# Kernel optimization log

Hardware: AMD Instinct MI355X
Metric: run time of the kernel (lower is better)

## Reference

```python
import jax, jax.numpy as jnp
import numpy as np

N_ATOMS = 4096
HSIZE = 128
N_HEADS = 8
D_K = HSIZE // N_HEADS


def setup_inputs() -> dict:
    key = jax.random.key(0)
    ks = jax.random.split(key, 11)
    s = 1.0 / np.sqrt(HSIZE)
    return {
        "query": jax.random.normal(ks[0], (N_ATOMS, HSIZE), dtype=jnp.float32),
        "key": jax.random.normal(ks[1], (N_ATOMS, HSIZE), dtype=jnp.float32),
        "value": jax.random.normal(ks[2], (N_ATOMS, HSIZE), dtype=jnp.float32),
        "mask": jax.random.randint(ks[3], (N_ATOMS, N_ATOMS), 0, 2, dtype=jnp.int32),
        "Wq": jax.random.normal(ks[4], (HSIZE, HSIZE), dtype=jnp.float32) * s,
        "bq": jnp.zeros((HSIZE,), dtype=jnp.float32),
        "Wk": jax.random.normal(ks[5], (HSIZE, HSIZE), dtype=jnp.float32) * s,
        "bk": jnp.zeros((HSIZE,), dtype=jnp.float32),
        "Wv": jax.random.normal(ks[6], (HSIZE, HSIZE), dtype=jnp.float32) * s,
        "bv": jnp.zeros((HSIZE,), dtype=jnp.float32),
        "Wo": jax.random.normal(ks[7], (HSIZE, HSIZE), dtype=jnp.float32) * s,
    }


def _mha(query, key, value, mask, Wq, bq, Wk, bk, Wv, bv, Wo):
    n = query.shape[0]
    # project and split heads: [n, hsize] -> [H, n, d_k]
    def heads(x, W, b):
        return (x @ W.T + b).reshape(n, N_HEADS, D_K).transpose(1, 0, 2)
    q = heads(query, Wq, bq)
    k = heads(key, Wk, bk)
    v = heads(value, Wv, bv)
    scale = 1.0 / jnp.sqrt(jnp.asarray(D_K, q.dtype))
    scores = jnp.einsum("hnd,hmd->hnm", q, k) * scale  # [H, n, n]
    scores = jnp.where(mask[None, :, :] == 0, jnp.asarray(-1e9, scores.dtype), scores)
    p_attn = jax.nn.softmax(scores, axis=-1)
    x = jnp.einsum("hnm,hmd->hnd", p_attn, v)  # [H, n, d_k]
    x = x.transpose(1, 0, 2).reshape(n, HSIZE)  # merge heads
    return x @ Wo.T  # output_linear has bias=False


def reference(query, key, value, mask, Wq, bq, Wk, bk, Wv, bv, Wo):
    return _mha(query, key, value, mask, Wq, bq, Wk, bk, Wv, bv, Wo)
```

## Files before the change

### kernel.cpp

```cpp
#include <hip/hip_runtime.h>

#define NA 4096
#define HS 128
#define CSTR 136

typedef unsigned short u16;
typedef unsigned long long u64;
using bf16x8  = __attribute__((ext_vector_type(8))) short;
using f32x4   = __attribute__((ext_vector_type(4))) float;
using ushort8 = __attribute__((ext_vector_type(8))) unsigned short;
using u32x4   = __attribute__((ext_vector_type(4))) unsigned;

#define QSCALE 0.18033688011112042f

static __device__ __forceinline__ u16 f2bf(float f) {
    unsigned u = __builtin_bit_cast(unsigned, f);
    u += 0x7FFFu + ((u >> 16) & 1u);
    return (u16)(u >> 16);
}

__global__ __launch_bounds__(256) void cvt_w(
    const float* __restrict__ Wq, const float* __restrict__ Wk,
    const float* __restrict__ Wv, const float* __restrict__ Wo,
    const float* __restrict__ bq, const float* __restrict__ bk,
    const float* __restrict__ bv,
    u16* __restrict__ Wf, float* __restrict__ bb)
{
    const int gid = blockIdx.x * 256 + threadIdx.x;
    const int e = gid * 4;
    const int mat = e >> 14, off = e & 16383;
    const float* src = (mat == 0) ? Wq : (mat == 1) ? Wk : (mat == 2) ? Wv : Wo;
    const float s = (mat == 0) ? QSCALE : 1.0f;
    float4 v = *(const float4*)(src + off);
    ushort4 o;
    o.x = f2bf(v.x * s); o.y = f2bf(v.y * s);
    o.z = f2bf(v.z * s); o.w = f2bf(v.w * s);
    const int j = off >> 7, k0 = off & 127;
    const int j0 = j >> 4, c = j & 15, kk = k0 >> 5, q = (k0 >> 3) & 3;
    const int tgt = mat * 16384 + ((j0 * 4 + kk) * 16 + c) * 32 + q * 8 + (k0 & 7);
    *(ushort4*)(Wf + tgt) = o;
    if (gid < 128)      bb[gid] = bq[gid] * QSCALE;
    else if (gid < 256) bb[gid] = bk[gid - 128];
    else if (gid < 384) bb[gid] = bv[gid - 256];
}

__global__ __launch_bounds__(256) void proj_mfma(
    const float* __restrict__ Xq, const float* __restrict__ Xk, const float* __restrict__ Xv,
    const u16* __restrict__ Wf, const float* __restrict__ bb,
    const int* __restrict__ mask,
    u16* __restrict__ Qbh, u16* __restrict__ Kbh, u16* __restrict__ VtB,
    u64* __restrict__ Mp)
{
    const int blk = blockIdx.x;
    const int t = threadIdx.x;

    if (blk >= 384) {
        const int mb = blk - 384;
        const int wv = t >> 6, lane = t & 63;
        const int row = mb * 4 + wv;
        const int* lp = mask + (size_t)row * NA + lane * 64;
        int4 v[16];
#pragma unroll
        for (int j = 0; j < 16; ++j) v[j] = *(const int4*)(lp + j * 4);
        u64 word = 0;
#pragma unroll
        for (int j = 0; j < 16; ++j) {
            const u64 nib = (u64)((v[j].x != 0 ? 1u : 0u) | (v[j].y != 0 ? 2u : 0u)
                                | (v[j].z != 0 ? 4u : 0u) | (v[j].w != 0 ? 8u : 0u));
            word |= nib << (4 * j);
        }
        Mp[(size_t)row * 64 + lane] = word;
        return;
    }

    const int mat = blk >> 7;
    const float* X = (mat == 0) ? Xq : (mat == 1) ? Xk : Xv;
    const u16* Wm = Wf + mat * 16384;
    const float* bm = bb + mat * 128;
    const int r0b = (blk & 127) * 32;

    __shared__ __align__(16) u16 Xs[32 * CSTR];
    __shared__ __align__(16) u16 Cs[32 * CSTR];

    {
        const int r = t >> 3, cb = (t & 7) * 16;
        const float* Xr = X + (size_t)(r0b + r) * HS + cb;
#pragma unroll
        for (int seg = 0; seg < 4; ++seg) {
            float4 f = *(const float4*)(Xr + seg * 4);
            ushort4 u;
            u.x = f2bf(f.x); u.y = f2bf(f.y); u.z = f2bf(f.z); u.w = f2bf(f.w);
            *(ushort4*)(Xs + r * CSTR + cb + seg * 4) = u;
        }
    }
    __syncthreads();

    const int wv = t >> 6, lane = t & 63;
    const int c = lane & 15, q = lane >> 4;
    const int rw = (wv & 1) * 16;
    const int j0b = (wv >> 1) * 4;

    bf16x8 af[4];
#pragma unroll
    for (int kk = 0; kk < 4; ++kk)
        af[kk] = *(const bf16x8*)(Xs + (rw + c) * CSTR + kk * 32 + q * 8);

    const f32x4 zero = {0.f, 0.f, 0.f, 0.f};
#pragma unroll
    for (int jj = 0; jj < 4; ++jj) {
        const int j0 = j0b + jj;
        f32x4 acc = zero;
#pragma unroll
        for (int kk = 0; kk < 4; ++kk) {
            bf16x8 bf = *(const bf16x8*)(Wm + (j0 * 4 + kk) * 512 + c * 32 + q * 8);
            acc = __builtin_amdgcn_mfma_f32_16x16x32_bf16(af[kk], bf, acc, 0, 0, 0);
        }
        const float bias = bm[j0 * 16 + c];
#pragma unroll
        for (int r = 0; r < 4; ++r)
            Cs[(rw + 4 * q + r) * CSTR + j0 * 16 + c] = f2bf(acc[r] + bias);
    }
    __syncthreads();

    if (mat < 2) {
        u16* dst = (mat == 0) ? Qbh : Kbh;
        const int h8 = t >> 5, r = t & 31;
        const u16* src = Cs + r * CSTR + h8 * 16;
        int drow = r0b + r;
        if (mat == 1) {
            const int k = (r0b & 32) + r;
            const int slot = ((k >> 5) * 2 + ((k >> 2) & 1)) * 16
                           + ((k >> 3) & 3) * 4 + (k & 3);
            drow = (r0b & ~63) + slot;
        }
        u16* dp = dst + (size_t)h8 * (NA * 16) + (size_t)drow * 16;
        *(bf16x8*)(dp)     = *(const bf16x8*)(src);
        *(bf16x8*)(dp + 8) = *(const bf16x8*)(src + 8);
    } else {
        const int d = t >> 1, s = t & 1;
        const int kb = r0b >> 6, ko = (r0b & 32) + s * 16;
        ushort8 v0, v1;
#pragma unroll
        for (int jj = 0; jj < 8; ++jj) v0[jj] = Cs[(s * 16 + jj) * CSTR + d];
#pragma unroll
        for (int jj = 0; jj < 8; ++jj) v1[jj] = Cs[(s * 16 + 8 + jj) * CSTR + d];
        u16* dp = VtB + (size_t)kb * 8192 + d * 64 + ko;
        *(ushort8*)(dp)     = v0;
        *(ushort8*)(dp + 8) = v1;
    }
}

__global__ __launch_bounds__(512, 4) void attn(
    const u64* __restrict__ Mp,
    const u16* __restrict__ Qbh, const u16* __restrict__ Kbh, const u16* __restrict__ VtB,
    float* __restrict__ part)
{
    __shared__ __align__(8)  u64 Mwp[16 * 17];
    __shared__ __align__(8)  u64 Mtab[16];

    const int t = threadIdx.x;
    const int h = t >> 6;
    const int lane = t & 63;
    const int c = lane & 15;
    const int q = lane >> 4;
    const int tile = blockIdx.x, split = blockIdx.y;
    const int i0 = tile * 16;
    const int kt0 = split * 1024;

    if (t < 256) {
        const int row = t >> 4, w = t & 15;
        Mwp[row * 17 + w] = Mp[(size_t)(i0 + row) * 64 + (kt0 >> 6) + w];
    }
    if (t < 16) {
        const unsigned lo = ((t & 1) ? 0xFFFFu : 0u) | ((t & 2) ? 0xFFFF0000u : 0u);
        const unsigned hi = ((t & 4) ? 0xFFFFu : 0u) | ((t & 8) ? 0xFFFF0000u : 0u);
        Mtab[t] = (u64)lo | ((u64)hi << 32);
    }

    const u16* Qh = Qbh + (size_t)h * (NA * 16);
    const u16* Kh = Kbh + (size_t)h * (NA * 16);

    const bf16x8 qf = *(const bf16x8*)(Qh + (size_t)(i0 + c) * 16 + (q & 1) * 8);

    bf16x8 ones;
#pragma unroll
    for (int i = 0; i < 8; ++i) ones[i] = (short)0x3F80;

    __syncthreads();

    const f32x4 zero = {0.f, 0.f, 0.f, 0.f};
    f32x4 Oacc = zero;
    f32x4 Lacc = zero;

    bf16x8 kf[4];
#pragma unroll
    for (int t4 = 0; t4 < 4; ++t4)
        kf[t4] = *(const bf16x8*)(Kh + (size_t)(kt0 + t4 * 16 + c) * 16 + (q & 1) * 8);

#pragma unroll 1
    for (int it = 0; it < 16; ++it) {
        const int kt = kt0 + it * 64;
        const u16* Vb = VtB + (size_t)(kt >> 6) * 8192 + (h * 16 + c) * 64;

        bf16x8 vf0 = *(const bf16x8*)(Vb + q * 8);
        bf16x8 vf1 = *(const bf16x8*)(Vb + 32 + q * 8);

        f32x4 ST[4];
        __builtin_amdgcn_s_setprio(1);
#pragma unroll
        for (int t4 = 0; t4 < 4; ++t4)
            ST[t4] = __builtin_amdgcn_mfma_f32_16x16x32_bf16(kf[t4], qf, zero, 0, 0, 0);
        __builtin_amdgcn_s_setprio(0);

        const int ktn = kt0 + ((it + 1) & 15) * 64;
#pragma unroll
        for (int t4 = 0; t4 < 4; ++t4)
            kf[t4] = *(const bf16x8*)(Kh + (size_t)(ktn + t4 * 16 + c) * 16 + (q & 1) * 8);

        const u64 w = Mwp[c * 17 + it];
        const unsigned wa = (unsigned)(w >> (8 * q));
        const unsigned wb = (unsigned)(w >> (32 + 8 * q));

        unsigned pl[4], ph[4];
#pragma unroll
        for (int t4 = 0; t4 < 4; ++t4) {
            const unsigned nib = (((t4 & 2) ? wb : wa) >> ((t4 & 1) * 4)) & 15u;
            float p0 = __builtin_amdgcn_exp2f(ST[t4][0]);
            float p1 = __builtin_amdgcn_exp2f(ST[t4][1]);
            float p2 = __builtin_amdgcn_exp2f(ST[t4][2]);
            float p3 = __builtin_amdgcn_exp2f(ST[t4][3]);
            unsigned lo, hi;
            asm("v_cvt_pk_bf16_f32 %0, %1, %2" : "=v"(lo) : "v"(p0), "v"(p1));
            asm("v_cvt_pk_bf16_f32 %0, %1, %2" : "=v"(hi) : "v"(p2), "v"(p3));
            const u64 mex = Mtab[nib];
            pl[t4] = lo & (unsigned)mex;
            ph[t4] = hi & (unsigned)(mex >> 32);
        }
        const u32x4 a0 = { pl[0], ph[0], pl[1], ph[1] };
        const u32x4 a1 = { pl[2], ph[2], pl[3], ph[3] };
        const bf16x8 pf0 = __builtin_bit_cast(bf16x8, a0);
        const bf16x8 pf1 = __builtin_bit_cast(bf16x8, a1);

        __builtin_amdgcn_s_setprio(1);
        Oacc = __builtin_amdgcn_mfma_f32_16x16x32_bf16(pf0, vf0, Oacc, 0, 0, 0);
        Oacc = __builtin_amdgcn_mfma_f32_16x16x32_bf16(pf1, vf1, Oacc, 0, 0, 0);
        Lacc = __builtin_amdgcn_mfma_f32_16x16x32_bf16(pf0, ones, Lacc, 0, 0, 0);
        Lacc = __builtin_amdgcn_mfma_f32_16x16x32_bf16(pf1, ones, Lacc, 0, 0, 0);
        __builtin_amdgcn_s_setprio(0);
    }

    float* base = part + (size_t)((tile * 4 + split) * 8 + h) * 272;
#pragma unroll
    for (int r = 0; r < 4; ++r)
        base[(4 * q + r) * 16 + c] = Oacc[r];
    if (c == 0) {
#pragma unroll
        for (int r = 0; r < 4; ++r)
            base[256 + 4 * q + r] = Lacc[r];
    }
}

__global__ __launch_bounds__(256) void reduce_out(
    const float* __restrict__ part, const u16* __restrict__ Wf,
    float* __restrict__ out)
{
    __shared__ __align__(16) u16 xs[16 * CSTR];

    const int t = threadIdx.x;
    const int tile = blockIdx.x;
    const int i0 = tile * 16;
    const float* Pt = part + (size_t)tile * 4 * 8 * 272;

    {
        const int i = t >> 4, d = t & 15;
#pragma unroll
        for (int h = 0; h < 8; ++h) {
            float os = 0.f, ls = 0.f;
#pragma unroll
            for (int s = 0; s < 4; ++s) {
                const float* b = Pt + (size_t)(s * 8 + h) * 272;
                os += b[i * 16 + d];
                ls += b[256 + i];
            }
            xs[i * CSTR + h * 16 + d] = f2bf(os / ls);
        }
    }
    __syncthreads();

    const int wv = t >> 6, lane = t & 63;
    const int c = lane & 15, q = lane >> 4;
    const u16* WoB = Wf + 3 * 16384;

    bf16x8 af[4];
#pragma unroll
    for (int kk = 0; kk < 4; ++kk)
        af[kk] = *(const bf16x8*)(xs + c * CSTR + kk * 32 + q * 8);

    const f32x4 zero = {0.f, 0.f, 0.f, 0.f};
#pragma unroll
    for (int jj = 0; jj < 2; ++jj) {
        const int j0 = wv * 2 + jj;
        f32x4 acc = zero;
#pragma unroll
        for (int kk = 0; kk < 4; ++kk) {
            bf16x8 bf = *(const bf16x8*)(WoB + (j0 * 4 + kk) * 512 + c * 32 + q * 8);
            acc = __builtin_amdgcn_mfma_f32_16x16x32_bf16(af[kk], bf, acc, 0, 0, 0);
        }
#pragma unroll
        for (int r = 0; r < 4; ++r)
            out[(size_t)(i0 + 4 * q + r) * HS + j0 * 16 + c] = acc[r];
    }
}

extern "C" void kernel_launch(void* const* d_in, const int* in_sizes, int n_in,
                              void* d_out, int out_size, void* d_ws, size_t ws_size,
                              hipStream_t stream) {
    const float* query = (const float*)d_in[0];
    const float* key   = (const float*)d_in[1];
    const float* value = (const float*)d_in[2];
    const int*   mask  = (const int*)d_in[3];
    const float* Wq    = (const float*)d_in[4];
    const float* bq    = (const float*)d_in[5];
    const float* Wk    = (const float*)d_in[6];
    const float* bk    = (const float*)d_in[7];
    const float* Wv    = (const float*)d_in[8];
    const float* bv    = (const float*)d_in[9];
    const float* Wo    = (const float*)d_in[10];

    u16* Qbh = (u16*)d_ws;
    u16* Kbh = Qbh + (size_t)NA * HS;
    u16* VtB = Kbh + (size_t)NA * HS;
    u16* Wf  = VtB + (size_t)NA * HS;
    float* bb    = (float*)(Wf + 4 * 16384);
    u64*  Mp    = (u64*)(bb + 384);
    float* partb = (float*)(Mp + (size_t)NA * 64);

    cvt_w<<<64, 256, 0, stream>>>(Wq, Wk, Wv, Wo, bq, bk, bv, Wf, bb);
    proj_mfma<<<384 + 1024, 256, 0, stream>>>(query, key, value, Wf, bb, mask,
                                              Qbh, Kbh, VtB, Mp);
    attn<<<dim3(256, 4), 512, 0, stream>>>(Mp, Qbh, Kbh, VtB, partb);
    reduce_out<<<256, 256, 0, stream>>>(partb, Wf, (float*)d_out);
}
```

Before: 173.8 us.

## Fuse weight conversion into projection and split-K reduce into attention

Removes the separate weight-conversion kernel: each projection block now converts its own Wq/Wk/Wv slice to bf16 in shared memory, and Wo is packed by extra blocks of the same launch. The reduce/output-projection kernel is folded into the attention kernel through an atomic counter per tile, so the last of the four split blocks combines the partials and applies Wo. This cuts the launch count from four to two. In exchange, every projection block redundantly reads and converts a full 128x128 weight, the attention blocks pay a fence and atomic, and the attention kernel uses more shared memory.

```diff
diff --git a/kernel.cpp b/kernel.cpp
--- a/kernel.cpp
+++ b/kernel.cpp
@@ -19,45 +19,21 @@
     return (u16)(u >> 16);
 }
 
-__global__ __launch_bounds__(256) void cvt_w(
+__global__ __launch_bounds__(256) void proj_pack(
+    const float* __restrict__ Xq, const float* __restrict__ Xk, const float* __restrict__ Xv,
     const float* __restrict__ Wq, const float* __restrict__ Wk,
     const float* __restrict__ Wv, const float* __restrict__ Wo,
     const float* __restrict__ bq, const float* __restrict__ bk,
-    const float* __restrict__ bv,
-    u16* __restrict__ Wf, float* __restrict__ bb)
-{
-    const int gid = blockIdx.x * 256 + threadIdx.x;
-    const int e = gid * 4;
-    const int mat = e >> 14, off = e & 16383;
-    const float* src = (mat == 0) ? Wq : (mat == 1) ? Wk : (mat == 2) ? Wv : Wo;
-    const float s = (mat == 0) ? QSCALE : 1.0f;
-    float4 v = *(const float4*)(src + off);
-    ushort4 o;
-    o.x = f2bf(v.x * s); o.y = f2bf(v.y * s);
-    o.z = f2bf(v.z * s); o.w = f2bf(v.w * s);
-    const int j = off >> 7, k0 = off & 127;
-    const int j0 = j >> 4, c = j & 15, kk = k0 >> 5, q = (k0 >> 3) & 3;
-    const int tgt = mat * 16384 + ((j0 * 4 + kk) * 16 + c) * 32 + q * 8 + (k0 & 7);
-    *(ushort4*)(Wf + tgt) = o;
-    if (gid < 128)      bb[gid] = bq[gid] * QSCALE;
-    else if (gid < 256) bb[gid] = bk[gid - 128];
-    else if (gid < 384) bb[gid] = bv[gid - 256];
-}
-
-__global__ __launch_bounds__(256) void proj_mfma(
-    const float* __restrict__ Xq, const float* __restrict__ Xk, const float* __restrict__ Xv,
-    const u16* __restrict__ Wf, const float* __restrict__ bb,
-    const int* __restrict__ mask,
+    const float* __restrict__ bv, const int* __restrict__ mask,
     u16* __restrict__ Qbh, u16* __restrict__ Kbh, u16* __restrict__ VtB,
-    u64* __restrict__ Mp)
+    u64* __restrict__ Mp, u16* __restrict__ WoF, int* __restrict__ cnt)
 {
     const int blk = blockIdx.x;
     const int t = threadIdx.x;
 
-    if (blk >= 384) {
-        const int mb = blk - 384;
+    if (blk < 1024) {
         const int wv = t >> 6, lane = t & 63;
-        const int row = mb * 4 + wv;
+        const int row = blk * 4 + wv;
         const int* lp = mask + (size_t)row * NA + lane * 64;
         int4 v[16];
 #pragma unroll
@@ -73,14 +49,48 @@
         return;
     }
 
-    const int mat = blk >> 7;
+    if (blk >= 1408) {
+        if (blk == 1424) {
+            if (t < 256) cnt[t] = 0;
+            return;
+        }
+        const int gid = (blk - 1408) * 256 + t;
+        const int off = gid * 4;
+        float4 v = *(const float4*)(Wo + off);
+        ushort4 o;
+        o.x = f2bf(v.x); o.y = f2bf(v.y); o.z = f2bf(v.z); o.w = f2bf(v.w);
+        const int j = off >> 7, k0 = off & 127;
+        const int j0 = j >> 4, c = j & 15, kk = k0 >> 5, q = (k0 >> 3) & 3;
+        *(ushort4*)(WoF + ((j0 * 4 + kk) * 16 + c) * 32 + q * 8 + (k0 & 7)) = o;
+        return;
+    }
+
+    const int pb = blk - 1024;
+    const int mat = pb >> 7;
     const float* X = (mat == 0) ? Xq : (mat == 1) ? Xk : Xv;
-    const u16* Wm = Wf + mat * 16384;
-    const float* bm = bb + mat * 128;
-    const int r0b = (blk & 127) * 32;
-
+    const float* Wsrc = (mat == 0) ? Wq : (mat == 1) ? Wk : Wv;
+    const float* bsrc = (mat == 0) ? bq : (mat == 1) ? bk : bv;
+    const float sc = (mat == 0) ? QSCALE : 1.0f;
+    const int r0b = (pb & 127) * 32;
+
+    __shared__ __align__(16) u16 Ws[16384];
     __shared__ __align__(16) u16 Xs[32 * CSTR];
     __shared__ __align__(16) u16 Cs[32 * CSTR];
+
+    {
+        const int base = t * 64;
+#pragma unroll
+        for (int i = 0; i < 16; ++i) {
+            const int off = base + i * 4;
+            float4 v = *(const float4*)(Wsrc + off);
+            ushort4 o;
+            o.x = f2bf(v.x * sc); o.y = f2bf(v.y * sc);
+            o.z = f2bf(v.z * sc); o.w = f2bf(v.w * sc);
+            const int j = off >> 7, k0 = off & 127;
+            const int j0 = j >> 4, c2 = j & 15, kk = k0 >> 5, qq = (k0 >> 3) & 3;
+            *(ushort4*)(Ws + (j0 * 4 + kk) * 512 + qq * 128 + c2 * 8 + (k0 & 7)) = o;
+        }
+    }
 
     {
         const int r = t >> 3, cb = (t & 7) * 16;
@@ -112,10 +122,10 @@
         f32x4 acc = zero;
 #pragma unroll
         for (int kk = 0; kk < 4; ++kk) {
-            bf16x8 bf = *(const bf16x8*)(Wm + (j0 * 4 + kk) * 512 + c * 32 + q * 8);
+            bf16x8 bf = *(const bf16x8*)(Ws + (j0 * 4 + kk) * 512 + q * 128 + c * 8);
             acc = __builtin_amdgcn_mfma_f32_16x16x32_bf16(af[kk], bf, acc, 0, 0, 0);
         }
-        const float bias = bm[j0 * 16 + c];
+        const float bias = bsrc[j0 * 16 + c] * sc;
 #pragma unroll
         for (int r = 0; r < 4; ++r)
             Cs[(rw + 4 * q + r) * CSTR + j0 * 16 + c] = f2bf(acc[r] + bias);
@@ -153,10 +163,13 @@
 __global__ __launch_bounds__(512, 4) void attn(
     const u64* __restrict__ Mp,
     const u16* __restrict__ Qbh, const u16* __restrict__ Kbh, const u16* __restrict__ VtB,
-    float* __restrict__ part)
+    const u16* __restrict__ WoF,
+    float* __restrict__ part, int* __restrict__ cnt, float* __restrict__ out)
 {
     __shared__ __align__(8)  u64 Mwp[16 * 17];
     __shared__ __align__(8)  u64 Mtab[16];
+    __shared__ int isLast;
+    __shared__ __align__(16) u16 xs[16 * CSTR];
 
     const int t = threadIdx.x;
     const int h = t >> 6;
@@ -258,58 +271,45 @@
         for (int r = 0; r < 4; ++r)
             base[256 + 4 * q + r] = Lacc[r];
     }
-}
-
-__global__ __launch_bounds__(256) void reduce_out(
-    const float* __restrict__ part, const u16* __restrict__ Wf,
-    float* __restrict__ out)
-{
-    __shared__ __align__(16) u16 xs[16 * CSTR];
-
-    const int t = threadIdx.x;
-    const int tile = blockIdx.x;
-    const int i0 = tile * 16;
+
+    __threadfence();
+    __syncthreads();
+    if (t == 0) isLast = (atomicAdd(&cnt[tile], 1) == 3);
+    __syncthreads();
+    if (!isLast) return;
+    __threadfence();
+
     const float* Pt = part + (size_t)tile * 4 * 8 * 272;
-
-    {
+    if (t < 256) {
         const int i = t >> 4, d = t & 15;
 #pragma unroll
-        for (int h = 0; h < 8; ++h) {
+        for (int hh = 0; hh < 8; ++hh) {
             float os = 0.f, ls = 0.f;
 #pragma unroll
             for (int s = 0; s < 4; ++s) {
-                const float* b = Pt + (size_t)(s * 8 + h) * 272;
+                const float* b = Pt + (size_t)(s * 8 + hh) * 272;
                 os += b[i * 16 + d];
                 ls += b[256 + i];
             }
-            xs[i * CSTR + h * 16 + d] = f2bf(os / ls);
-        }
-    }
-    __syncthreads();
-
-    const int wv = t >> 6, lane = t & 63;
-    const int c = lane & 15, q = lane >> 4;
-    const u16* WoB = Wf + 3 * 16384;
+            xs[i * CSTR + hh * 16 + d] = f2bf(os / ls);
+        }
+    }
+    __syncthreads();
 
     bf16x8 af[4];
 #pragma unroll
     for (int kk = 0; kk < 4; ++kk)
         af[kk] = *(const bf16x8*)(xs + c * CSTR + kk * 32 + q * 8);
 
-    const f32x4 zero = {0.f, 0.f, 0.f, 0.f};
-#pragma unroll
-    for (int jj = 0; jj < 2; ++jj) {
-        const int j0 = wv * 2 + jj;
-        f32x4 acc = zero;
-#pragma unroll
-        for (int kk = 0; kk < 4; ++kk) {
-            bf16x8 bf = *(const bf16x8*)(WoB + (j0 * 4 + kk) * 512 + c * 32 + q * 8);
-            acc = __builtin_amdgcn_mfma_f32_16x16x32_bf16(af[kk], bf, acc, 0, 0, 0);
-        }
-#pragma unroll
-        for (int r = 0; r < 4; ++r)
-            out[(size_t)(i0 + 4 * q + r) * HS + j0 * 16 + c] = acc[r];
-    }
+    f32x4 acc = zero;
+#pragma unroll
+    for (int kk = 0; kk < 4; ++kk) {
+        bf16x8 bf = *(const bf16x8*)(WoF + (h * 4 + kk) * 512 + c * 32 + q * 8);
+        acc = __builtin_amdgcn_mfma_f32_16x16x32_bf16(af[kk], bf, acc, 0, 0, 0);
+    }
+#pragma unroll
+    for (int r = 0; r < 4; ++r)
+        out[(size_t)(i0 + 4 * q + r) * HS + h * 16 + c] = acc[r];
 }
 
 extern "C" void kernel_launch(void* const* d_in, const int* in_sizes, int n_in,
@@ -330,14 +330,14 @@
     u16* Qbh = (u16*)d_ws;
     u16* Kbh = Qbh + (size_t)NA * HS;
     u16* VtB = Kbh + (size_t)NA * HS;
-    u16* Wf  = VtB + (size_t)NA * HS;
-    float* bb    = (float*)(Wf + 4 * 16384);
-    u64*  Mp    = (u64*)(bb + 384);
-    float* partb = (float*)(Mp + (size_t)NA * 64);
-
-    cvt_w<<<64, 256, 0, stream>>>(Wq, Wk, Wv, Wo, bq, bk, bv, Wf, bb);
-    proj_mfma<<<384 + 1024, 256, 0, stream>>>(query, key, value, Wf, bb, mask,
-                                              Qbh, Kbh, VtB, Mp);
-    attn<<<dim3(256, 4), 512, 0, stream>>>(Mp, Qbh, Kbh, VtB, partb);
-    reduce_out<<<256, 256, 0, stream>>>(partb, Wf, (float*)d_out);
+    u16* WoF = VtB + (size_t)NA * HS;
+    u64*  Mp  = (u64*)(WoF + 16384);
+    int*  cnt = (int*)(Mp + (size_t)NA * 64);
+    float* partb = (float*)(cnt + 256);
+
+    proj_pack<<<1425, 256, 0, stream>>>(query, key, value, Wq, Wk, Wv, Wo,
+                                        bq, bk, bv, mask,
+                                        Qbh, Kbh, VtB, Mp, WoF, cnt);
+    attn<<<dim3(256, 4), 512, 0, stream>>>(Mp, Qbh, Kbh, VtB, WoF,
+                                           partb, cnt, (float*)d_out);
 }
```

Result: slower. 386.1 us (+122.1%).
